# Kernel optimization log

Hardware: AMD Instinct MI355X
Metric: run time of the kernel (lower is better)

Reference implementation:

```python
import jax, jax.numpy as jnp
import numpy as np

B, S, D, H = 2, 2048, 1024, 16
DK = D // H
SCALE = 1.0 / np.sqrt(DK).astype(np.float32)


def setup_inputs() -> dict:
    key = jax.random.key(0)
    ks = jax.random.split(key, 7)
    std = 1.0 / np.sqrt(D).astype(np.float32)
    return {
        "query": jax.random.normal(ks[0], (B, S, D), jnp.float32),
        "key": jax.random.normal(ks[1], (B, S, D), jnp.float32),
        "value": jax.random.normal(ks[2], (B, S, D), jnp.float32),
        "Wq": jax.random.normal(ks[3], (D, D), jnp.float32) * std,
        "Wk": jax.random.normal(ks[4], (D, D), jnp.float32) * std,
        "Wv": jax.random.normal(ks[5], (D, D), jnp.float32) * std,
        "Wo": jax.random.normal(ks[6], (D, D), jnp.float32) * std,
    }


def _split_heads(x):
    # [B, S, D] -> [B, H, S, DK]
    return x.reshape(B, S, H, DK).transpose(0, 2, 1, 3)


def reference(query, key, value, Wq, Wk, Wv, Wo):
    Q = _split_heads(query @ Wq)
    K = _split_heads(key @ Wk)
    V = _split_heads(value @ Wv)
    # explicit full-score attention, as in the original (mask=None, dropout off)
    scores = jnp.einsum("bhqd,bhkd->bhqk", Q, K) * SCALE
    attn = jax.nn.softmax(scores, axis=-1)
    out = jnp.einsum("bhqk,bhkd->bhqd", attn, V)
    out = out.transpose(0, 2, 1, 3).reshape(B, S, D)  # merge heads
    return out @ Wo
```

## Files before the change

kernel.cpp:

```cpp
#include <hip/hip_runtime.h>

#define B_ 2
#define S_ 2048
#define D_ 1024
#define H_ 16

typedef unsigned short u16;
typedef unsigned long long u64;
typedef __bf16 bf16x8 __attribute__((ext_vector_type(8)));
typedef float f32x4 __attribute__((ext_vector_type(4)));
typedef unsigned short u16x8 __attribute__((ext_vector_type(8)));
typedef unsigned short u16x4 __attribute__((ext_vector_type(4)));
typedef unsigned uint4v __attribute__((ext_vector_type(4)));

__device__ __forceinline__ unsigned swz128(unsigned o) {
  return o ^ (((o >> 7) & 7) << 4);
}
__device__ __forceinline__ unsigned swz256(unsigned o) {
  return o ^ (((o >> 8) & 7) << 4);
}

__device__ __forceinline__ unsigned xcd_swz(unsigned id, unsigned cpx) {
  return (id & 7) * cpx + (id >> 3);
}

__device__ __forceinline__ void gload_lds16(const void* g, void* l) {
  __builtin_amdgcn_global_load_lds(
      (const __attribute__((address_space(1))) unsigned*)g,
      (__attribute__((address_space(3))) unsigned*)l, 16, 0, 0);
}

__device__ __forceinline__ u16 f2bf(float f) {
  union { float f; unsigned u; } v;
  v.f = f;
  unsigned u = v.u;
  return (u16)((u + 0x7fffu + ((u >> 16) & 1u)) >> 16);
}

__device__ __forceinline__ unsigned cvtpk(float lo, float hi) {
  unsigned d;
  asm("v_cvt_pk_bf16_f32 %0, %1, %2" : "=v"(d) : "v"(lo), "v"(hi));
  return d;
}

struct T4 { const float* in[4]; u16* out[4]; };
__global__ __launch_bounds__(256) void transpose_w4(T4 p) {
  __shared__ u16 t[64][65];
  const float* in = p.in[blockIdx.z];
  u16* out = p.out[blockIdx.z];
  int r0 = blockIdx.y * 64, c0 = blockIdx.x * 64;
  for (int i = threadIdx.x; i < 4096; i += 256) {
    int r = i >> 6, c = i & 63;
    t[r][c] = f2bf(in[(size_t)(r0 + r) * 1024 + c0 + c]);
  }
  __syncthreads();
  for (int i = threadIdx.x; i < 4096; i += 256) {
    int r = i >> 6, c = i & 63;
    out[(size_t)(c0 + r) * 1024 + r0 + c] = t[c][r];
  }
}

struct QKV { const float* A[3]; const u16* BT[3]; u16* C[2]; u16* VT; };
__global__ __launch_bounds__(256) void gemm_qkv(QKV p) {
  constexpr int K = 1024, N = 1024;
  __shared__ __align__(16) u16 lbuf[2][128 * 64];
  const int tid = threadIdx.x, lane = tid & 63, w = tid >> 6;
  const int wr = w >> 1, wc = w & 1;
  const int z = blockIdx.z;
  const int m0 = blockIdx.x * 128, n0 = blockIdx.y * 128;
  const int g = lane >> 4, c16 = lane & 15;
  f32x4 acc[4][4] = {};
  const float* Af = p.A[z] + (size_t)m0 * K;
  const char* Bb = (const char*)(p.BT[z] + (size_t)n0 * K);
  char* lAb = (char*)lbuf[0];
  char* lBb = (char*)lbuf[1];
  for (int kt = 0; kt < K; kt += 64) {
    for (int c = 0; c < 4; ++c) {
      unsigned o = c * 4096 + tid * 16;
      unsigned u = swz128(o);
      gload_lds16(Bb + (size_t)(u >> 7) * (K * 2) + kt * 2 + (u & 127), lBb + o);
    }
    for (int c = 0; c < 4; ++c) {
      unsigned o = c * 4096 + tid * 16;
      unsigned row = o >> 7, kc = (o & 127) >> 1;
      const float* s = Af + (size_t)row * K + kt + kc;
      float4 f0 = *(const float4*)s;
      float4 f1 = *(const float4*)(s + 4);
      uint4v d;
      d[0] = cvtpk(f0.x, f0.y);
      d[1] = cvtpk(f0.z, f0.w);
      d[2] = cvtpk(f1.x, f1.y);
      d[3] = cvtpk(f1.z, f1.w);
      *(uint4v*)(lAb + swz128(o)) = d;
    }
    asm volatile("s_waitcnt vmcnt(0)" ::: "memory");
    __syncthreads();
    for (int ks = 0; ks < 2; ++ks) {
      bf16x8 af[4], bf[4];
      for (int i = 0; i < 4; ++i) {
        unsigned row = wr * 64 + i * 16 + c16;
        unsigned o = row * 128 + ks * 64 + g * 16;
        af[i] = *(const bf16x8*)(lAb + (o ^ ((row & 7) << 4)));
      }
      for (int j = 0; j < 4; ++j) {
        unsigned row = wc * 64 + j * 16 + c16;
        unsigned o = row * 128 + ks * 64 + g * 16;
        bf[j] = *(const bf16x8*)(lBb + (o ^ ((row & 7) << 4)));
      }
      for (int i = 0; i < 4; ++i)
        for (int j = 0; j < 4; ++j)
          acc[i][j] = __builtin_amdgcn_mfma_f32_16x16x32_bf16(af[i], bf[j],
                                                              acc[i][j], 0, 0, 0);
    }
    __syncthreads();
  }
  if (z < 2) {
    u16* C = p.C[z];
    for (int i = 0; i < 4; ++i)
      for (int j = 0; j < 4; ++j) {
        int row = m0 + wr * 64 + i * 16 + g * 4;
        int col = n0 + wc * 64 + j * 16 + c16;
        for (int r = 0; r < 4; ++r)
          C[(size_t)(row + r) * N + col] = f2bf(acc[i][j][r]);
      }
  } else {
    char* Tb = (char*)lbuf;
    for (int i = 0; i < 4; ++i)
      for (int j = 0; j < 4; ++j) {
        unsigned s_local = wr * 64 + i * 16 + g * 4;
        unsigned dk_col = wc * 64 + j * 16 + c16;
        unsigned o = dk_col * 256 + s_local * 2;
        u16x4 ov;
        ov[0] = f2bf(acc[i][j][0]);
        ov[1] = f2bf(acc[i][j][1]);
        ov[2] = f2bf(acc[i][j][2]);
        ov[3] = f2bf(acc[i][j][3]);
        *(u16x4*)(Tb + swz256(o)) = ov;
      }
    __syncthreads();
    const int b = m0 >> 11, s0blk = m0 & 2047;
    for (int c = 0; c < 8; ++c) {
      unsigned idx = c * 4096 + tid * 16;
      unsigned row = idx >> 8, off = idx & 255;
      int h = (n0 + (int)row) >> 6, dk = (n0 + (int)row) & 63;
      int bh = b * 16 + h;
      char* dst = (char*)p.VT + (((size_t)bh * 64 + dk) * S_ + s0blk) * 2 + off;
      *(u16x8*)dst = *(const u16x8*)(Tb + swz256(idx));
    }
  }
}

__global__ __launch_bounds__(256) void gemm_bt_f32(const u16* __restrict__ A,
                                                   const u16* __restrict__ BT,
                                                   float* __restrict__ C) {
  constexpr int K = 1024, N = 1024;
  __shared__ __align__(16) u16 lA[128 * 64];
  __shared__ __align__(16) u16 lB[64 * 64];
  const int tid = threadIdx.x, lane = tid & 63, w = tid >> 6;
  const int wr = w >> 1, wc = w & 1;
  const int m0 = blockIdx.x * 128, n0 = blockIdx.y * 64;
  const int g = lane >> 4, c16 = lane & 15;
  f32x4 acc[4][2] = {};
  const char* Ab = (const char*)(A + (size_t)m0 * K);
  const char* Bb = (const char*)(BT + (size_t)n0 * K);
  char* lAb = (char*)lA;
  char* lBb = (char*)lB;
  for (int kt = 0; kt < K; kt += 64) {
    for (int c = 0; c < 4; ++c) {
      unsigned o = w * 4096 + c * 1024 + lane * 16;
      unsigned u = swz128(o);
      gload_lds16(Ab + (size_t)(u >> 7) * (K * 2) + kt * 2 + (u & 127),
                  lAb + w * 4096 + c * 1024);
    }
    for (int c = 0; c < 2; ++c) {
      unsigned o = w * 2048 + c * 1024 + lane * 16;
      unsigned u = swz128(o);
      gload_lds16(Bb + (size_t)(u >> 7) * (K * 2) + kt * 2 + (u & 127),
                  lBb + w * 2048 + c * 1024);
    }
    asm volatile("s_waitcnt vmcnt(0)" ::: "memory");
    __syncthreads();
    for (int ks = 0; ks < 2; ++ks) {
      bf16x8 af[4], bf[2];
      for (int i = 0; i < 4; ++i) {
        unsigned row = wr * 64 + i * 16 + c16;
        unsigned o = row * 128 + ks * 64 + g * 16;
        af[i] = *(const bf16x8*)(lAb + (o ^ ((row & 7) << 4)));
      }
      for (int j = 0; j < 2; ++j) {
        unsigned row = wc * 32 + j * 16 + c16;
        unsigned o = row * 128 + ks * 64 + g * 16;
        bf[j] = *(const bf16x8*)(lBb + (o ^ ((row & 7) << 4)));
      }
      for (int i = 0; i < 4; ++i)
        for (int j = 0; j < 2; ++j)
          acc[i][j] = __builtin_amdgcn_mfma_f32_16x16x32_bf16(af[i], bf[j],
                                                              acc[i][j], 0, 0, 0);
    }
    __syncthreads();
  }
  for (int i = 0; i < 4; ++i)
    for (int j = 0; j < 2; ++j) {
      int row = m0 + wr * 64 + i * 16 + g * 4;
      int col = n0 + wc * 32 + j * 16 + c16;
      for (int r = 0; r < 4; ++r)
        C[(size_t)(row + r) * N + col] = acc[i][j][r];
    }
}

__global__ __launch_bounds__(256) void flash_attn(const u16* __restrict__ Q,
                                                  const u16* __restrict__ K,
                                                  const u16* __restrict__ VT,
                                                  u16* __restrict__ O) {
  __shared__ __align__(16) u16 lP[64 * 64];
  __shared__ __align__(16) u16 lK[2][64 * 64];
  __shared__ __align__(16) u16 lV[2][64 * 64];
  const int tid = threadIdx.x, lane = tid & 63, w = tid >> 6;
  const int g = lane >> 4, c16 = lane & 15;
  unsigned id = blockIdx.x + blockIdx.y * gridDim.x;
  unsigned sw = xcd_swz(id, 128);
  const int q0 = (sw & 31) * 64;
  const int bh = sw >> 5, b = bh >> 4, h = bh & 15;
  const char* Qb = (const char*)(Q + (size_t)(b * S_ + q0) * D_ + h * 64);
  const char* Kb = (const char*)(K + (size_t)b * S_ * D_ + h * 64);
  const char* Vb = (const char*)(VT + (size_t)bh * 64 * S_);
  char* lPb = (char*)lP;
  char* lKb = (char*)lK;
  char* lVb = (char*)lV;

  for (int c = 0; c < 2; ++c) {
    unsigned o = w * 2048 + c * 1024 + lane * 16;
    unsigned u = swz128(o);
    gload_lds16(Qb + (size_t)(u >> 7) * (D_ * 2) + (u & 127), lPb + w * 2048 + c * 1024);
    gload_lds16(Kb + (size_t)(u >> 7) * (D_ * 2) + (u & 127), lKb + w * 2048 + c * 1024);
    gload_lds16(Vb + (size_t)(u >> 7) * (S_ * 2) + (u & 127), lVb + w * 2048 + c * 1024);
  }
  float m_run = -INFINITY, l_run = 0.f;
  f32x4 oacc[4] = {};
  asm volatile("s_waitcnt vmcnt(0)" ::: "memory");
  __syncthreads();
  bf16x8 qf[2];
  {
    unsigned row = w * 16 + c16;
    for (int ks = 0; ks < 2; ++ks) {
      unsigned o = row * 128 + ks * 64 + g * 16;
      qf[ks] = *(const bf16x8*)(lPb + swz128(o));
    }
  }
  const float SC2 = 0.125f * 1.44269504088896340736f;
  int cur = 0;
  for (int kv0 = 0; kv0 < S_; kv0 += 64, cur ^= 1) {
    char* curK = lKb + cur * 8192;
    char* curV = lVb + cur * 8192;
    if (kv0 + 64 < S_) {
      char* nK = lKb + (cur ^ 1) * 8192;
      char* nV = lVb + (cur ^ 1) * 8192;
      for (int c = 0; c < 2; ++c) {
        unsigned o = w * 2048 + c * 1024 + lane * 16;
        unsigned u = swz128(o);
        gload_lds16(Kb + (size_t)(kv0 + 64 + (u >> 7)) * (D_ * 2) + (u & 127),
                    nK + w * 2048 + c * 1024);
        gload_lds16(Vb + (size_t)(u >> 7) * (S_ * 2) + (size_t)(kv0 + 64) * 2 + (u & 127),
                    nV + w * 2048 + c * 1024);
      }
    }
    f32x4 s[4] = {};
    __builtin_amdgcn_s_setprio(1);
    for (int ks = 0; ks < 2; ++ks)
      for (int j = 0; j < 4; ++j) {
        unsigned row = j * 16 + c16;
        unsigned o = row * 128 + ks * 64 + g * 16;
        bf16x8 kf = *(const bf16x8*)(curK + swz128(o));
        s[j] = __builtin_amdgcn_mfma_f32_16x16x32_bf16(kf, qf[ks], s[j], 0, 0, 0);
      }
    __builtin_amdgcn_s_setprio(0);
    float rm = s[0][0];
    for (int j = 0; j < 4; ++j)
      for (int r = 0; r < 4; ++r) rm = fmaxf(rm, s[j][r]);
    rm = fmaxf(rm, __shfl_xor(rm, 16));
    rm = fmaxf(rm, __shfl_xor(rm, 32));
    if (!__all((rm - m_run) * SC2 <= 8.0f)) {
      float mn = fmaxf(m_run, rm);
      float sc = exp2f((m_run - mn) * SC2);
      l_run *= sc;
      for (int i = 0; i < 4; ++i) oacc[i] *= sc;
      m_run = mn;
    }
    float rs = 0.f;
    unsigned qrow = w * 16 + c16;
    for (int j = 0; j < 4; ++j) {
      float p0 = exp2f((s[j][0] - m_run) * SC2);
      float p1 = exp2f((s[j][1] - m_run) * SC2);
      float p2 = exp2f((s[j][2] - m_run) * SC2);
      float p3 = exp2f((s[j][3] - m_run) * SC2);
      rs += (p0 + p1) + (p2 + p3);
      unsigned w0 = cvtpk(p0, p1);
      unsigned w1 = cvtpk(p2, p3);
      unsigned o = qrow * 128 + (unsigned)(j * 16 + g * 4) * 2;
      *(u64*)(lPb + swz128(o)) = (u64)w0 | ((u64)w1 << 32);
    }
    rs += __shfl_xor(rs, 16);
    rs += __shfl_xor(rs, 32);
    l_run += rs;
    __builtin_amdgcn_s_setprio(1);
    for (int ks = 0; ks < 2; ++ks) {
      unsigned po = qrow * 128 + ks * 64 + g * 16;
      bf16x8 pf = *(const bf16x8*)(lPb + swz128(po));
      for (int i = 0; i < 4; ++i) {
        unsigned vo = (unsigned)(i * 16 + c16) * 128 + ks * 64 + g * 16;
        bf16x8 vf = *(const bf16x8*)(curV + swz128(vo));
        oacc[i] = __builtin_amdgcn_mfma_f32_16x16x32_bf16(vf, pf, oacc[i], 0, 0, 0);
      }
    }
    __builtin_amdgcn_s_setprio(0);
    asm volatile("s_waitcnt vmcnt(0)" ::: "memory");
    __syncthreads();
  }
  float inv = 1.f / l_run;
  int q = q0 + w * 16 + c16;
  u16* orow = O + (size_t)(b * S_ + q) * D_ + h * 64;
  for (int i = 0; i < 4; ++i) {
    unsigned e0 = cvtpk(oacc[i][0] * inv, oacc[i][1] * inv);
    unsigned e1 = cvtpk(oacc[i][2] * inv, oacc[i][3] * inv);
    *(u64*)(orow + i * 16 + g * 4) = (u64)e0 | ((u64)e1 << 32);
  }
}

extern "C" void kernel_launch(void* const* d_in, const int* in_sizes, int n_in,
                              void* d_out, int out_size, void* d_ws, size_t ws_size,
                              hipStream_t stream) {
  const float* q_in = (const float*)d_in[0];
  const float* k_in = (const float*)d_in[1];
  const float* v_in = (const float*)d_in[2];
  const float* Wq = (const float*)d_in[3];
  const float* Wk = (const float*)d_in[4];
  const float* Wv = (const float*)d_in[5];
  const float* Wo = (const float*)d_in[6];
  u16* ws = (u16*)d_ws;
  const size_t WSZ = (size_t)1024 * 1024;
  const size_t TSZ = (size_t)B_ * S_ * D_;
  u16* WqT = ws;
  u16* WkT = ws + WSZ;
  u16* WvT = ws + 2 * WSZ;
  u16* WoT = ws + 3 * WSZ;
  u16* Qb = ws + 4 * WSZ;
  u16* Kb = Qb + TSZ;
  u16* VTb = Kb + TSZ;
  u16* Ob = VTb + TSZ;
  dim3 tb(256);
  T4 tw = {{Wq, Wk, Wv, Wo}, {WqT, WkT, WvT, WoT}};
  transpose_w4<<<dim3(16, 16, 4), tb, 0, stream>>>(tw);
  QKV gq = {{q_in, k_in, v_in}, {WqT, WkT, WvT}, {Qb, Kb}, VTb};
  gemm_qkv<<<dim3(32, 8, 3), tb, 0, stream>>>(gq);
  flash_attn<<<dim3(32, 32), tb, 0, stream>>>(Qb, Kb, VTb, Ob);
  gemm_bt_f32<<<dim3(32, 16), tb, 0, stream>>>(Ob, WoT, (float*)d_out);
}
```

Baseline: 156.2 us.

## Widen output GEMM tile to 128x128 and precompute flash-attention LDS offsets

The output projection GEMM now uses 128x128 tiles instead of 128x64, which doubles per-wave accumulators and halves the grid so each A tile is reused across more columns. In flash attention, swizzled LDS addresses are precomputed once per thread, the row max uses v_max3 instructions, and the row-sum accumulation is split into independent partial sums. These aim to cut address arithmetic and VALU work in the inner loop. The GEMM change raises register use and reduces the block count to 256, which may lower occupancy.

Measured after the change: 160.2 us. 2.6% more time.

```diff
diff --git a/kernel.cpp b/kernel.cpp
--- a/kernel.cpp
+++ b/kernel.cpp
@@ -40,6 +40,12 @@
 __device__ __forceinline__ unsigned cvtpk(float lo, float hi) {
   unsigned d;
   asm("v_cvt_pk_bf16_f32 %0, %1, %2" : "=v"(d) : "v"(lo), "v"(hi));
+  return d;
+}
+
+__device__ __forceinline__ float max3f(float a, float b, float c) {
+  float d;
+  asm("v_max3_f32 %0, %1, %2, %3" : "=v"(d) : "v"(a), "v"(b), "v"(c));
   return d;
 }
 
@@ -155,54 +161,48 @@
                                                    float* __restrict__ C) {
   constexpr int K = 1024, N = 1024;
   __shared__ __align__(16) u16 lA[128 * 64];
-  __shared__ __align__(16) u16 lB[64 * 64];
+  __shared__ __align__(16) u16 lB[128 * 64];
   const int tid = threadIdx.x, lane = tid & 63, w = tid >> 6;
   const int wr = w >> 1, wc = w & 1;
-  const int m0 = blockIdx.x * 128, n0 = blockIdx.y * 64;
+  const int m0 = blockIdx.x * 128, n0 = blockIdx.y * 128;
   const int g = lane >> 4, c16 = lane & 15;
-  f32x4 acc[4][2] = {};
+  f32x4 acc[4][4] = {};
   const char* Ab = (const char*)(A + (size_t)m0 * K);
   const char* Bb = (const char*)(BT + (size_t)n0 * K);
   char* lAb = (char*)lA;
   char* lBb = (char*)lB;
   for (int kt = 0; kt < K; kt += 64) {
     for (int c = 0; c < 4; ++c) {
-      unsigned o = w * 4096 + c * 1024 + lane * 16;
+      unsigned o = c * 4096 + tid * 16;
       unsigned u = swz128(o);
-      gload_lds16(Ab + (size_t)(u >> 7) * (K * 2) + kt * 2 + (u & 127),
-                  lAb + w * 4096 + c * 1024);
-    }
-    for (int c = 0; c < 2; ++c) {
-      unsigned o = w * 2048 + c * 1024 + lane * 16;
-      unsigned u = swz128(o);
-      gload_lds16(Bb + (size_t)(u >> 7) * (K * 2) + kt * 2 + (u & 127),
-                  lBb + w * 2048 + c * 1024);
+      gload_lds16(Ab + (size_t)(u >> 7) * (K * 2) + kt * 2 + (u & 127), lAb + o);
+      gload_lds16(Bb + (size_t)(u >> 7) * (K * 2) + kt * 2 + (u & 127), lBb + o);
     }
     asm volatile("s_waitcnt vmcnt(0)" ::: "memory");
     __syncthreads();
     for (int ks = 0; ks < 2; ++ks) {
-      bf16x8 af[4], bf[2];
+      bf16x8 af[4], bf[4];
       for (int i = 0; i < 4; ++i) {
         unsigned row = wr * 64 + i * 16 + c16;
         unsigned o = row * 128 + ks * 64 + g * 16;
         af[i] = *(const bf16x8*)(lAb + (o ^ ((row & 7) << 4)));
       }
-      for (int j = 0; j < 2; ++j) {
-        unsigned row = wc * 32 + j * 16 + c16;
+      for (int j = 0; j < 4; ++j) {
+        unsigned row = wc * 64 + j * 16 + c16;
         unsigned o = row * 128 + ks * 64 + g * 16;
         bf[j] = *(const bf16x8*)(lBb + (o ^ ((row & 7) << 4)));
       }
       for (int i = 0; i < 4; ++i)
-        for (int j = 0; j < 2; ++j)
+        for (int j = 0; j < 4; ++j)
           acc[i][j] = __builtin_amdgcn_mfma_f32_16x16x32_bf16(af[i], bf[j],
                                                               acc[i][j], 0, 0, 0);
     }
     __syncthreads();
   }
   for (int i = 0; i < 4; ++i)
-    for (int j = 0; j < 2; ++j) {
+    for (int j = 0; j < 4; ++j) {
       int row = m0 + wr * 64 + i * 16 + g * 4;
-      int col = n0 + wc * 32 + j * 16 + c16;
+      int col = n0 + wc * 64 + j * 16 + c16;
       for (int r = 0; r < 4; ++r)
         C[(size_t)(row + r) * N + col] = acc[i][j][r];
     }
@@ -228,55 +228,63 @@
   char* lKb = (char*)lK;
   char* lVb = (char*)lV;
 
+  const unsigned mask = (c16 & 7) << 4;
+  const unsigned fb0 = c16 * 128 + ((g * 16) ^ mask);
+  const unsigned fb1 = c16 * 128 + ((64 + g * 16) ^ mask);
+  unsigned uo[2];
+  for (int c = 0; c < 2; ++c) uo[c] = swz128(w * 2048 + c * 1024 + lane * 16);
+
   for (int c = 0; c < 2; ++c) {
-    unsigned o = w * 2048 + c * 1024 + lane * 16;
-    unsigned u = swz128(o);
-    gload_lds16(Qb + (size_t)(u >> 7) * (D_ * 2) + (u & 127), lPb + w * 2048 + c * 1024);
-    gload_lds16(Kb + (size_t)(u >> 7) * (D_ * 2) + (u & 127), lKb + w * 2048 + c * 1024);
-    gload_lds16(Vb + (size_t)(u >> 7) * (S_ * 2) + (u & 127), lVb + w * 2048 + c * 1024);
+    unsigned u = uo[c];
+    char* dst = (char*)(w * 2048 + c * 1024);
+    gload_lds16(Qb + (size_t)(u >> 7) * (D_ * 2) + (u & 127), lPb + (size_t)dst);
+    gload_lds16(Kb + (size_t)(u >> 7) * (D_ * 2) + (u & 127), lKb + (size_t)dst);
+    gload_lds16(Vb + (size_t)(u >> 7) * (S_ * 2) + (u & 127), lVb + (size_t)dst);
   }
   float m_run = -INFINITY, l_run = 0.f;
   f32x4 oacc[4] = {};
   asm volatile("s_waitcnt vmcnt(0)" ::: "memory");
   __syncthreads();
   bf16x8 qf[2];
-  {
-    unsigned row = w * 16 + c16;
-    for (int ks = 0; ks < 2; ++ks) {
-      unsigned o = row * 128 + ks * 64 + g * 16;
-      qf[ks] = *(const bf16x8*)(lPb + swz128(o));
-    }
-  }
+  qf[0] = *(const bf16x8*)(lPb + w * 2048 + fb0);
+  qf[1] = *(const bf16x8*)(lPb + w * 2048 + fb1);
   const float SC2 = 0.125f * 1.44269504088896340736f;
+  const unsigned qrow = w * 16 + c16;
+  const unsigned pw = qrow * 128 + ((g * 8) ^ (mask & 16));
+  const unsigned mh = mask & 96;
   int cur = 0;
   for (int kv0 = 0; kv0 < S_; kv0 += 64, cur ^= 1) {
-    char* curK = lKb + cur * 8192;
-    char* curV = lVb + cur * 8192;
+    const char* curK = lKb + cur * 8192;
+    const char* curV = lVb + cur * 8192;
     if (kv0 + 64 < S_) {
       char* nK = lKb + (cur ^ 1) * 8192;
       char* nV = lVb + (cur ^ 1) * 8192;
       for (int c = 0; c < 2; ++c) {
-        unsigned o = w * 2048 + c * 1024 + lane * 16;
-        unsigned u = swz128(o);
+        unsigned u = uo[c];
+        unsigned dst = w * 2048 + c * 1024;
         gload_lds16(Kb + (size_t)(kv0 + 64 + (u >> 7)) * (D_ * 2) + (u & 127),
-                    nK + w * 2048 + c * 1024);
+                    nK + dst);
         gload_lds16(Vb + (size_t)(u >> 7) * (S_ * 2) + (size_t)(kv0 + 64) * 2 + (u & 127),
-                    nV + w * 2048 + c * 1024);
+                    nV + dst);
       }
     }
     f32x4 s[4] = {};
     __builtin_amdgcn_s_setprio(1);
-    for (int ks = 0; ks < 2; ++ks)
-      for (int j = 0; j < 4; ++j) {
-        unsigned row = j * 16 + c16;
-        unsigned o = row * 128 + ks * 64 + g * 16;
-        bf16x8 kf = *(const bf16x8*)(curK + swz128(o));
-        s[j] = __builtin_amdgcn_mfma_f32_16x16x32_bf16(kf, qf[ks], s[j], 0, 0, 0);
-      }
+    for (int j = 0; j < 4; ++j) {
+      bf16x8 kf = *(const bf16x8*)(curK + fb0 + j * 2048);
+      s[j] = __builtin_amdgcn_mfma_f32_16x16x32_bf16(kf, qf[0], s[j], 0, 0, 0);
+    }
+    for (int j = 0; j < 4; ++j) {
+      bf16x8 kf = *(const bf16x8*)(curK + fb1 + j * 2048);
+      s[j] = __builtin_amdgcn_mfma_f32_16x16x32_bf16(kf, qf[1], s[j], 0, 0, 0);
+    }
     __builtin_amdgcn_s_setprio(0);
-    float rm = s[0][0];
-    for (int j = 0; j < 4; ++j)
-      for (int r = 0; r < 4; ++r) rm = fmaxf(rm, s[j][r]);
+    float t0 = max3f(s[0][0], s[0][1], s[0][2]);
+    float t1 = max3f(s[0][3], s[1][0], s[1][1]);
+    float t2 = max3f(s[1][2], s[1][3], s[2][0]);
+    float t3 = max3f(s[2][1], s[2][2], s[2][3]);
+    float t4 = max3f(s[3][0], s[3][1], s[3][2]);
+    float rm = fmaxf(max3f(t0, t1, t2), max3f(t3, t4, s[3][3]));
     rm = fmaxf(rm, __shfl_xor(rm, 16));
     rm = fmaxf(rm, __shfl_xor(rm, 32));
     if (!__all((rm - m_run) * SC2 <= 8.0f)) {
@@ -286,30 +294,32 @@
       for (int i = 0; i < 4; ++i) oacc[i] *= sc;
       m_run = mn;
     }
-    float rs = 0.f;
-    unsigned qrow = w * 16 + c16;
+    float rsj[4];
     for (int j = 0; j < 4; ++j) {
       float p0 = exp2f((s[j][0] - m_run) * SC2);
       float p1 = exp2f((s[j][1] - m_run) * SC2);
       float p2 = exp2f((s[j][2] - m_run) * SC2);
       float p3 = exp2f((s[j][3] - m_run) * SC2);
-      rs += (p0 + p1) + (p2 + p3);
+      rsj[j] = (p0 + p1) + (p2 + p3);
       unsigned w0 = cvtpk(p0, p1);
       unsigned w1 = cvtpk(p2, p3);
-      unsigned o = qrow * 128 + (unsigned)(j * 16 + g * 4) * 2;
-      *(u64*)(lPb + swz128(o)) = (u64)w0 | ((u64)w1 << 32);
-    }
+      *(u64*)(lPb + pw + ((unsigned)(j * 32) ^ mh)) = (u64)w0 | ((u64)w1 << 32);
+    }
+    float rs = (rsj[0] + rsj[1]) + (rsj[2] + rsj[3]);
     rs += __shfl_xor(rs, 16);
     rs += __shfl_xor(rs, 32);
     l_run += rs;
     __builtin_amdgcn_s_setprio(1);
-    for (int ks = 0; ks < 2; ++ks) {
-      unsigned po = qrow * 128 + ks * 64 + g * 16;
-      bf16x8 pf = *(const bf16x8*)(lPb + swz128(po));
+    {
+      bf16x8 pf0 = *(const bf16x8*)(lPb + w * 2048 + fb0);
       for (int i = 0; i < 4; ++i) {
-        unsigned vo = (unsigned)(i * 16 + c16) * 128 + ks * 64 + g * 16;
-        bf16x8 vf = *(const bf16x8*)(curV + swz128(vo));
-        oacc[i] = __builtin_amdgcn_mfma_f32_16x16x32_bf16(vf, pf, oacc[i], 0, 0, 0);
+        bf16x8 vf = *(const bf16x8*)(curV + fb0 + i * 2048);
+        oacc[i] = __builtin_amdgcn_mfma_f32_16x16x32_bf16(vf, pf0, oacc[i], 0, 0, 0);
+      }
+      bf16x8 pf1 = *(const bf16x8*)(lPb + w * 2048 + fb1);
+      for (int i = 0; i < 4; ++i) {
+        bf16x8 vf = *(const bf16x8*)(curV + fb1 + i * 2048);
+        oacc[i] = __builtin_amdgcn_mfma_f32_16x16x32_bf16(vf, pf1, oacc[i], 0, 0, 0);
       }
     }
     __builtin_amdgcn_s_setprio(0);
@@ -353,5 +363,5 @@
   QKV gq = {{q_in, k_in, v_in}, {WqT, WkT, WvT}, {Qb, Kb}, VTb};
   gemm_qkv<<<dim3(32, 8, 3), tb, 0, stream>>>(gq);
   flash_attn<<<dim3(32, 32), tb, 0, stream>>>(Qb, Kb, VTb, Ob);
-  gemm_bt_f32<<<dim3(32, 16), tb, 0, stream>>>(Ob, WoT, (float*)d_out);
-}
+  gemm_bt_f32<<<dim3(32, 8), tb, 0, stream>>>(Ob, WoT, (float*)d_out);
+}
```
